# Kernel tuning notes

Measured on AMD Instinct MI355X. Metric: run time of the kernel, lower is better.

The kernel has to match this reference:

```python
import jax, jax.numpy as jnp
import numpy as np

RHO = 1e-8
EPS = 1e-8
THRESH = 0.9
MARK = -2


def maxi(x):
    # keep only the max entry along last dim, zero elsewhere
    idx = jnp.argmax(x, axis=-1, keepdims=True)
    return jnp.where(jnp.arange(x.shape[-1]) == idx, x, 0.0)


def argmaxi(x, eps=EPS):
    mx = jnp.abs(maxi(x))
    factors = jnp.max(mx, axis=-1, keepdims=True) - eps
    return mx / factors


def outer_forward(mm0, xs, rho=RHO):
    # mm0: (fields, mems, dim), xs: (batch, fields, dim)
    m = mm0 - 0.5
    x = xs - 0.5
    num = jnp.einsum('fmd,bfd->bfm', m, x) * 0.5
    m_norm = jnp.sqrt(jnp.sum(m * m, axis=-1))            # (f, m)
    x_norm = jnp.sqrt(jnp.sum(x * x, axis=-1))[..., None]  # (b, f, 1)
    return num / (m_norm[None] * x_norm + rho) + 0.5


def hidden_forward(mm, child_x, rho=RHO):
    # mm: (nodes, children, h_mems, c_mems), child_x: (batch, nodes*children, c_mems)
    n, c, hm, cm = mm.shape
    b = child_x.shape[0]
    x = maxi(child_x).reshape(b, n, c, cm)
    prop = jnp.einsum('nchk,bnck->bnh', mm, x)
    x_norm = jnp.sqrt(jnp.sum(x * x, axis=(2, 3)))[..., None]  # (b, n, 1)
    return prop / (c * x_norm + rho)


def mark_reserved_indices(acts, usages, trigger, mark=MARK):
    # acts: (b, n, m); usages: (n, m); trigger: (b, n, 1)
    res = jnp.argsort(acts, axis=-1)[:, :, -1:]        # argmax index, (b, n, 1)
    res = jnp.where(trigger, -1, res)
    res = res[:, :, 0].T                               # (n, b)
    sort_indices = jnp.argsort(usages, axis=-1)        # (n, m) ascending usage
    mask = res != -1                                   # (n, b)
    matches = ((res[:, :, None] == sort_indices[:, None, :]) & mask[:, :, None]).any(axis=1)  # (n, m)
    return jnp.where(matches, mark, sort_indices), sort_indices


def move_value_to_back(x, value=MARK):
    order = jnp.argsort((x == value).astype(jnp.int32), axis=-1)  # stable sort
    return jnp.take_along_axis(x, order, axis=-1)


def expand_for_batches(x, batch_size):
    n, m = x.shape
    full = batch_size // m + 1
    tiled = jnp.broadcast_to(x[None], (full, n, m)).transpose(1, 0, 2).reshape(n, -1)
    return tiled[:, :batch_size]


def growth_argmaxi(x, counts, eps=EPS, threshold=THRESH):
    b, n, m = x.shape
    normal = argmaxi(x, eps)
    trigger = jnp.sum(x > threshold, axis=-1, keepdims=True) <= 0  # (b, n, 1)
    avail, allidx = mark_reserved_indices(normal, counts, trigger, MARK)
    avail = move_value_to_back(avail, MARK)
    avail = expand_for_batches(avail, b)
    allidx = expand_for_batches(allidx, b)
    final = jnp.where(avail == MARK, allidx, avail)  # (n, b)
    idx = final.T.reshape(b, n, 1)
    vals = jnp.take_along_axis(x, idx, axis=-1)
    vals = jnp.where(vals == 0, 1.0, vals)
    gp = jnp.where(jnp.arange(m) == idx, vals, 0.0)  # scatter into zeros
    gp = argmaxi(jnp.abs(gp), eps)
    grown = jnp.where(trigger, gp, normal)
    uc = jnp.sum(grown, axis=0)
    uc = jnp.where(uc <= 0, counts, uc)
    return grown, uc


def setup_inputs() -> dict:
    key = jax.random.key(0)
    k1, k2, k3, k4 = jax.random.split(key, 4)
    xs = jax.random.uniform(k1, (32, 4096, 64), dtype=jnp.float32)
    mm0 = jax.random.uniform(k2, (4096, 64, 64), dtype=jnp.float32)
    mm1 = jax.random.normal(k3, (512, 8, 64, 64), dtype=jnp.float32) * 0.1
    mm2 = jax.random.normal(k4, (64, 8, 64, 64), dtype=jnp.float32) * 0.1
    counts = jnp.ones((64, 64), dtype=jnp.float32)
    return {'xs': xs, 'mm0': mm0, 'mm1': mm1, 'mm2': mm2, 'counts': counts}


def reference(xs, mm0, mm1, mm2, counts):
    h0 = outer_forward(mm0, xs)      # (b, 4096, 64)
    h1 = hidden_forward(mm1, h0)     # (b, 512, 64)
    h2 = hidden_forward(mm2, h1)     # (b, 64, 64)
    grown, _ = growth_argmaxi(h2, counts)
    return grown
```

## Files before the change

### kernel.cpp

```cpp
#include <hip/hip_runtime.h>
#include <cstdint>
#include <cstddef>

#define RHO 1e-8f
#define EPSV 1e-8f
#define THRESH 0.9f

typedef float v2f __attribute__((ext_vector_type(2)));

__device__ __forceinline__ float wave_max(float v) {
#pragma unroll
  for (int off = 1; off < 64; off <<= 1) v = fmaxf(v, __shfl_xor(v, off, 64));
  return v;
}

__device__ __forceinline__ void lds_barrier() {
  asm volatile("s_waitcnt lgkmcnt(0)" ::: "memory");
  __builtin_amdgcn_sched_barrier(0);
  __builtin_amdgcn_s_barrier();
  __builtin_amdgcn_sched_barrier(0);
}

__global__ __launch_bounds__(128) void stage1_kernel(
    const float* __restrict__ xs, const float* __restrict__ mm0,
    float* __restrict__ maxv1, int* __restrict__ idx1) {
  const int tid = threadIdx.x;
  const int lane = tid & 63;
  const int wave = tid >> 6;
  const int f = blockIdx.x;
  const int mg = lane >> 3, bg = lane & 7;
  const int mrow0 = wave * 32 + mg;

  __shared__ float bestS[2][32];
  __shared__ int bidxS[2][32];

  const float* mb = mm0 + (size_t)f * 4096 + (size_t)mrow0 * 64;
  const float* xb = xs + (size_t)f * 64 + (size_t)bg * (4096 * 64);

  v2f acc[4][4][2];
  v2f na[4], nx[4];
#pragma unroll
  for (int i = 0; i < 4; ++i) {
    na[i] = (v2f){0.f, 0.f};
    nx[i] = (v2f){0.f, 0.f};
#pragma unroll
    for (int j = 0; j < 4; ++j) {
      acc[i][j][0] = (v2f){0.f, 0.f};
      acc[i][j][1] = (v2f){0.f, 0.f};
    }
  }

#pragma clang loop unroll_count(2)
  for (int q = 0; q < 16; ++q) {
    float4 a[4], bx[4];
#pragma unroll
    for (int i = 0; i < 4; ++i) {
      float4 v = *reinterpret_cast<const float4*>(mb + i * (8 * 64) + 4 * q);
      a[i] = (float4){v.x - 0.5f, v.y - 0.5f, v.z - 0.5f, v.w - 0.5f};
    }
#pragma unroll
    for (int j = 0; j < 4; ++j) {
      float4 v = *reinterpret_cast<const float4*>(
          xb + (size_t)j * (8 * 4096 * 64) + 4 * q);
      bx[j] = (float4){v.x - 0.5f, v.y - 0.5f, v.z - 0.5f, v.w - 0.5f};
    }
#pragma unroll
    for (int i = 0; i < 4; ++i) {
      na[i] = (v2f){a[i].x, a[i].y} * (v2f){a[i].x, a[i].y} + na[i];
      na[i] = (v2f){a[i].z, a[i].w} * (v2f){a[i].z, a[i].w} + na[i];
    }
#pragma unroll
    for (int j = 0; j < 4; ++j) {
      nx[j] = (v2f){bx[j].x, bx[j].y} * (v2f){bx[j].x, bx[j].y} + nx[j];
      nx[j] = (v2f){bx[j].z, bx[j].w} * (v2f){bx[j].z, bx[j].w} + nx[j];
    }
#pragma unroll
    for (int i = 0; i < 4; ++i)
#pragma unroll
      for (int j = 0; j < 4; ++j) {
        acc[i][j][0] = (v2f){a[i].x, a[i].y} * (v2f){bx[j].x, bx[j].y} + acc[i][j][0];
        acc[i][j][1] = (v2f){a[i].z, a[i].w} * (v2f){bx[j].z, bx[j].w} + acc[i][j][1];
      }
  }

  float mn_i[4], xn_j[4];
#pragma unroll
  for (int i = 0; i < 4; ++i) mn_i[i] = sqrtf(na[i].x + na[i].y);
#pragma unroll
  for (int j = 0; j < 4; ++j) xn_j[j] = sqrtf(nx[j].x + nx[j].y);

  float best[4];
  int bidx[4];
#pragma unroll
  for (int j = 0; j < 4; ++j) { best[j] = -__builtin_inff(); bidx[j] = 0; }
#pragma unroll
  for (int i = 0; i < 4; ++i)
#pragma unroll
    for (int j = 0; j < 4; ++j) {
      const float dot =
          acc[i][j][0].x + acc[i][j][0].y + acc[i][j][1].x + acc[i][j][1].y;
      const float val = (dot * 0.5f) / (mn_i[i] * xn_j[j] + RHO) + 0.5f;
      if (val > best[j]) { best[j] = val; bidx[j] = mrow0 + 8 * i; }
    }
#pragma unroll
  for (int off = 8; off < 64; off <<= 1) {
#pragma unroll
    for (int j = 0; j < 4; ++j) {
      const float pv = __shfl_xor(best[j], off, 64);
      const int pm = __shfl_xor(bidx[j], off, 64);
      if (pv > best[j] || (pv == best[j] && pm < bidx[j])) {
        best[j] = pv; bidx[j] = pm;
      }
    }
  }
  if (mg == 0) {
#pragma unroll
    for (int j = 0; j < 4; ++j) {
      bestS[wave][bg + 8 * j] = best[j];
      bidxS[wave][bg + 8 * j] = bidx[j];
    }
  }
  __syncthreads();
  if (tid < 32) {
    const float v0 = bestS[0][tid], v1 = bestS[1][tid];
    const int i0 = bidxS[0][tid], i1 = bidxS[1][tid];
    const bool take1 = (v1 > v0);
    maxv1[f * 32 + tid] = take1 ? v1 : v0;
    idx1[f * 32 + tid] = take1 ? i1 : i0;
  }
}

#define STAGE_WRITE(T, R)                                    \
  do {                                                       \
    _Pragma("unroll") for (int i_ = 0; i_ < 4; ++i_) {       \
      const int g_ = tid + 256 * i_;                         \
      const int h_ = g_ >> 4, k0_ = (g_ & 15) * 4;           \
      (T)[(k0_ + 0) * 64 + (h_ ^ (k0_ + 0))] = (R)[i_].x;    \
      (T)[(k0_ + 1) * 64 + (h_ ^ (k0_ + 1))] = (R)[i_].y;    \
      (T)[(k0_ + 2) * 64 + (h_ ^ (k0_ + 2))] = (R)[i_].z;    \
      (T)[(k0_ + 3) * 64 + (h_ ^ (k0_ + 3))] = (R)[i_].w;    \
    }                                                        \
  } while (0)

#define LOAD_CHILD(R, C)                                     \
  do {                                                       \
    _Pragma("unroll") for (int i_ = 0; i_ < 4; ++i_)         \
        (R)[i_] = src[(C) * 1024 + tid + 256 * i_];          \
  } while (0)

#define COMPUTE_CHILD(C, T)                                              \
  do {                                                                   \
    _Pragma("unroll") for (int i_ = 0; i_ < 8; ++i_) {                   \
      const int b_ = wave * 8 + i_;                                      \
      const int k_ = ixL[(C) * 32 + b_];                                 \
      const float v_ = mvL[(C) * 32 + b_];                               \
      const float w_ = (T)[k_ * 64 + (lane ^ k_)];                       \
      acc[i_] = fmaf(w_, v_, acc[i_]);                                   \
      s2[i_] = fmaf(v_, v_, s2[i_]);                                     \
    }                                                                    \
  } while (0)

#define PIPELINE_MATMUL()                        \
  do {                                           \
    float4 rE[4], rO[4];                         \
    LOAD_CHILD(rE, 0);                           \
    LOAD_CHILD(rO, 1);                           \
    STAGE_WRITE(tA, rE);                         \
    lds_barrier();                               \
    _Pragma("unroll") for (int cc = 0; cc < 8; cc += 2) { \
      if (cc + 2 < 8) LOAD_CHILD(rE, cc + 2);    \
      COMPUTE_CHILD(cc, tA);                     \
      STAGE_WRITE(tB, rO);                       \
      lds_barrier();                             \
      if (cc + 3 < 8) LOAD_CHILD(rO, cc + 3);    \
      COMPUTE_CHILD(cc + 1, tB);                 \
      if (cc + 2 < 8) { STAGE_WRITE(tA, rE); }   \
      lds_barrier();                             \
    }                                            \
  } while (0)

__global__ __launch_bounds__(256) void stage2_kernel(
    const float* __restrict__ maxv_in, const int* __restrict__ idx_in,
    const float* __restrict__ mm,
    float* __restrict__ maxv_out, int* __restrict__ idx_out) {
  const int node = blockIdx.x;
  const int lane = threadIdx.x & 63;
  const int wave = threadIdx.x >> 6;
  const int tid = threadIdx.x;

  __shared__ float tA[4096], tB[4096];
  __shared__ float mvL[256];
  __shared__ int ixL[256];

  const float4* src = reinterpret_cast<const float4*>(mm + (size_t)node * (8 * 4096));

  mvL[tid] = maxv_in[node * 256 + tid];
  ixL[tid] = idx_in[node * 256 + tid];

  float acc[8], s2[8];
#pragma unroll
  for (int i = 0; i < 8; ++i) { acc[i] = 0.f; s2[i] = 0.f; }

  PIPELINE_MATMUL();

#pragma unroll
  for (int i = 0; i < 8; ++i) {
    const int b = wave * 8 + i;
    const float val = acc[i] / (8.f * sqrtf(s2[i]) + RHO);
    const float mx = wave_max(val);
    unsigned long long t = __ballot(val == mx);
    int j0 = __ffsll((long long)t) - 1;
    if (lane == 0) {
      maxv_out[node * 32 + b] = mx;
      idx_out[node * 32 + b] = j0;
    }
  }
}

__global__ __launch_bounds__(256) void grow_kernel(
    const float* __restrict__ maxv_in, const int* __restrict__ idx_in,
    const float* __restrict__ mm,
    const float* __restrict__ counts, float* __restrict__ out) {
  const int node = blockIdx.x;
  const int lane = threadIdx.x & 63;
  const int wave = threadIdx.x >> 6;
  const int tid = threadIdx.x;

  __shared__ float tA[4096], tB[4096];
  __shared__ float mvL[256];
  __shared__ int ixL[256];
  __shared__ float hbuf[32 * 64];
  __shared__ float mxvS[32];
  __shared__ int idxS[32];
  __shared__ int trgS[32];
  __shared__ float cntS[64];
  __shared__ int sidxS[64];
  __shared__ int flagS[64];
  __shared__ int compS[64];
  __shared__ int selS[32];
  __shared__ float valS[32];
  __shared__ int keptS[1];

  const float4* src = reinterpret_cast<const float4*>(mm + (size_t)node * (8 * 4096));

  mvL[tid] = maxv_in[node * 256 + tid];
  ixL[tid] = idx_in[node * 256 + tid];

  float acc[8], s2[8];
#pragma unroll
  for (int i = 0; i < 8; ++i) { acc[i] = 0.f; s2[i] = 0.f; }

  PIPELINE_MATMUL();

#pragma unroll
  for (int i = 0; i < 8; ++i) {
    const int b = wave * 8 + i;
    const float val = acc[i] / (8.f * sqrtf(s2[i]) + RHO);
    const float mx = wave_max(val);
    unsigned long long t = __ballot(val == mx);
    int j0 = __ffsll((long long)t) - 1;
    hbuf[b * 64 + lane] = val;
    unsigned long long big = __ballot(val > THRESH);
    if (lane == 0) {
      mxvS[b] = mx; idxS[b] = j0; trgS[b] = (big == 0ULL) ? 1 : 0;
    }
  }

  if (tid < 64) { cntS[tid] = counts[node * 64 + tid]; flagS[tid] = 0; }
  __syncthreads();
  if (tid < 64) {
    float cl = cntS[tid];
    int rank = 0;
    for (int j = 0; j < 64; ++j) {
      float cj = cntS[j];
      rank += (cj < cl || (cj == cl && j < tid)) ? 1 : 0;
    }
    sidxS[rank] = tid;
  }
  __syncthreads();
  if (tid < 32) {
    const int b = tid;
    if (!trgS[b]) {
      int j = idxS[b];
      float a = fabsf(mxvS[b]);
      int res;
      if (a > EPSV) res = j;
      else if (a == 0.f) res = 63;
      else if (a == EPSV) res = j;
      else res = (j == 63) ? 62 : 63;
      flagS[res] = 1;
    }
  }
  __syncthreads();
  if (wave == 0) {
    int s = sidxS[lane];
    int keep = flagS[s] ? 0 : 1;
    unsigned long long kb = __ballot(keep);
    int pos = __popcll(kb & ((1ULL << lane) - 1ULL));
    if (keep) compS[pos] = s;
    if (lane == 0) keptS[0] = __popcll(kb);
  }
  __syncthreads();
  if (tid < 32) {
    const int b = tid;
    int fin = (b < keptS[0]) ? compS[b] : sidxS[b];
    int idxb; float a;
    if (trgS[b]) {
      idxb = fin;
      float v = hbuf[b * 64 + idxb];
      if (v == 0.f) v = 1.f;
      a = fabsf(v);
    } else {
      idxb = idxS[b];
      a = fabsf(mxvS[b]);
    }
    selS[b] = idxb;
    valS[b] = a / (a - EPSV);
  }
  __syncthreads();
#pragma unroll
  for (int r = 0; r < 8; ++r) {
    int i = tid + 256 * r;
    int b = i >> 6, h = i & 63;
    out[((size_t)b * 64 + node) * 64 + h] = (h == selS[b]) ? valS[b] : 0.f;
  }
}

extern "C" void kernel_launch(void* const* d_in, const int* in_sizes, int n_in,
                              void* d_out, int out_size, void* d_ws, size_t ws_size,
                              hipStream_t stream) {
  const float* xs = (const float*)d_in[0];
  const float* mm0 = (const float*)d_in[1];
  const float* mm1 = (const float*)d_in[2];
  const float* mm2 = (const float*)d_in[3];
  const float* counts = (const float*)d_in[4];
  float* out = (float*)d_out;
  char* ws = (char*)d_ws;

  float* maxv1 = (float*)(ws + 0);
  int* idx1 = (int*)(ws + 524288);
  float* maxv2 = (float*)(ws + 1048576);
  int* idx2 = (int*)(ws + 1114112);

  stage1_kernel<<<dim3(4096), dim3(128), 0, stream>>>(xs, mm0, maxv1, idx1);
  stage2_kernel<<<dim3(512), dim3(256), 0, stream>>>(maxv1, idx1, mm1, maxv2, idx2);
  grow_kernel<<<dim3(64), dim3(256), 0, stream>>>(maxv2, idx2, mm2, counts, out);
}
```

Measured before the change: 247.3 us.

## Stage mm0 and xs through swizzled LDS with register prefetch, four fields per block

Stage1 now processes four fields per block. For each field it copies the 64x64 mm0 tile and the 32x64 xs slice into XOR-swizzled shared memory, with the next field's tiles prefetched into registers and double-buffered so global loads overlap compute. Previously each thread read its operands straight from global memory with strided float4 loads. The per-block argmax reduction is also remapped so each wave owns 16 batches and writes results directly, removing the cross-wave LDS merge. This costs more LDS (about 24KB), more registers, extra barriers, and four times fewer blocks.

```diff
diff --git a/kernel.cpp b/kernel.cpp
--- a/kernel.cpp
+++ b/kernel.cpp
@@ -27,107 +27,181 @@
   const int tid = threadIdx.x;
   const int lane = tid & 63;
   const int wave = tid >> 6;
-  const int f = blockIdx.x;
-  const int mg = lane >> 3, bg = lane & 7;
-  const int mrow0 = wave * 32 + mg;
-
-  __shared__ float bestS[2][32];
-  __shared__ int bidxS[2][32];
-
-  const float* mb = mm0 + (size_t)f * 4096 + (size_t)mrow0 * 64;
-  const float* xb = xs + (size_t)f * 64 + (size_t)bg * (4096 * 64);
-
-  v2f acc[4][4][2];
-  v2f na[4], nx[4];
-#pragma unroll
-  for (int i = 0; i < 4; ++i) {
-    na[i] = (v2f){0.f, 0.f};
-    nx[i] = (v2f){0.f, 0.f};
+  const int mg = lane & 15, bg = lane >> 4;
+
+  __shared__ float mS[2][4096];
+  __shared__ float xS[2048];
+
+  const int f0 = blockIdx.x * 4;
+
+  float4 Rm[8], Rx[4];
+
+#define S1_LOADM(F)                                                      \
+  do {                                                                   \
+    const float* mf_ = mm0 + (size_t)(F)*4096;                           \
+    _Pragma("unroll") for (int i_ = 0; i_ < 8; ++i_) {                   \
+      const int g_ = tid + 128 * i_;                                     \
+      Rm[i_] = *reinterpret_cast<const float4*>(mf_ + g_ * 4);           \
+    }                                                                    \
+  } while (0)
+
+#define S1_LOADX(F)                                                      \
+  do {                                                                   \
+    _Pragma("unroll") for (int i_ = 0; i_ < 4; ++i_) {                   \
+      const int g_ = tid + 128 * i_;                                     \
+      const int b_ = g_ >> 4, q_ = g_ & 15;                              \
+      Rx[i_] = *reinterpret_cast<const float4*>(                         \
+          xs + ((size_t)b_ * 4096 + (F)) * 64 + q_ * 4);                 \
+    }                                                                    \
+  } while (0)
+
+#define S1_WRITEM(P)                                                     \
+  do {                                                                   \
+    _Pragma("unroll") for (int i_ = 0; i_ < 8; ++i_) {                   \
+      const int g_ = tid + 128 * i_;                                     \
+      const int r_ = g_ >> 4, q_ = g_ & 15;                              \
+      float4 w_ = {Rm[i_].x - 0.5f, Rm[i_].y - 0.5f, Rm[i_].z - 0.5f,    \
+                   Rm[i_].w - 0.5f};                                     \
+      *reinterpret_cast<float4*>(                                        \
+          &mS[P][(r_ * 16 + (q_ ^ (r_ & 15))) * 4]) = w_;                \
+    }                                                                    \
+  } while (0)
+
+#define S1_WRITEX()                                                      \
+  do {                                                                   \
+    _Pragma("unroll") for (int i_ = 0; i_ < 4; ++i_) {                   \
+      const int g_ = tid + 128 * i_;                                     \
+      const int b_ = g_ >> 4, q_ = g_ & 15;                              \
+      float4 w_ = {Rx[i_].x - 0.5f, Rx[i_].y - 0.5f, Rx[i_].z - 0.5f,    \
+                   Rx[i_].w - 0.5f};                                     \
+      *reinterpret_cast<float4*>(                                        \
+          &xS[(b_ * 16 + (q_ ^ (b_ & 15))) * 4]) = w_;                   \
+    }                                                                    \
+  } while (0)
+
+  S1_LOADM(f0);
+  S1_LOADX(f0);
+  S1_WRITEM(0);
+  S1_WRITEX();
+  S1_LOADM(f0 + 1);
+  S1_LOADX(f0 + 1);
+  lds_barrier();
+
+#pragma unroll
+  for (int k = 0; k < 4; ++k) {
+    const int f = f0 + k;
+    const float* mT = mS[k & 1];
+
+    v2f acc[4][4][2];
+    v2f na[4], nx[4];
+#pragma unroll
+    for (int i = 0; i < 4; ++i) {
+      na[i] = (v2f){0.f, 0.f};
+      nx[i] = (v2f){0.f, 0.f};
+#pragma unroll
+      for (int j = 0; j < 4; ++j) {
+        acc[i][j][0] = (v2f){0.f, 0.f};
+        acc[i][j][1] = (v2f){0.f, 0.f};
+      }
+    }
+
+#pragma unroll
+    for (int q = 0; q < 16; ++q) {
+      float4 a[4], bx[4];
+#pragma unroll
+      for (int i = 0; i < 4; ++i) {
+        const int r = mg + 16 * i;
+        a[i] = *reinterpret_cast<const float4*>(
+            &mT[(r * 16 + (q ^ (r & 15))) * 4]);
+      }
+#pragma unroll
+      for (int j = 0; j < 4; ++j) {
+        const int b = wave * 16 + bg + 4 * j;
+        bx[j] = *reinterpret_cast<const float4*>(
+            &xS[(b * 16 + (q ^ (b & 15))) * 4]);
+      }
+#pragma unroll
+      for (int i = 0; i < 4; ++i) {
+        na[i] = (v2f){a[i].x, a[i].y} * (v2f){a[i].x, a[i].y} + na[i];
+        na[i] = (v2f){a[i].z, a[i].w} * (v2f){a[i].z, a[i].w} + na[i];
+      }
+#pragma unroll
+      for (int j = 0; j < 4; ++j) {
+        nx[j] = (v2f){bx[j].x, bx[j].y} * (v2f){bx[j].x, bx[j].y} + nx[j];
+        nx[j] = (v2f){bx[j].z, bx[j].w} * (v2f){bx[j].z, bx[j].w} + nx[j];
+      }
+#pragma unroll
+      for (int i = 0; i < 4; ++i)
+#pragma unroll
+        for (int j = 0; j < 4; ++j) {
+          acc[i][j][0] =
+              (v2f){a[i].x, a[i].y} * (v2f){bx[j].x, bx[j].y} + acc[i][j][0];
+          acc[i][j][1] =
+              (v2f){a[i].z, a[i].w} * (v2f){bx[j].z, bx[j].w} + acc[i][j][1];
+        }
+    }
+
+    if (k < 3) S1_WRITEM((k + 1) & 1);
+
+    float mn_i[4], xn_j[4];
+#pragma unroll
+    for (int i = 0; i < 4; ++i) mn_i[i] = sqrtf(na[i].x + na[i].y);
+#pragma unroll
+    for (int j = 0; j < 4; ++j) xn_j[j] = sqrtf(nx[j].x + nx[j].y);
+
+    float best[4];
+    int bidx[4];
 #pragma unroll
     for (int j = 0; j < 4; ++j) {
-      acc[i][j][0] = (v2f){0.f, 0.f};
-      acc[i][j][1] = (v2f){0.f, 0.f};
-    }
-  }
-
-#pragma clang loop unroll_count(2)
-  for (int q = 0; q < 16; ++q) {
-    float4 a[4], bx[4];
-#pragma unroll
-    for (int i = 0; i < 4; ++i) {
-      float4 v = *reinterpret_cast<const float4*>(mb + i * (8 * 64) + 4 * q);
-      a[i] = (float4){v.x - 0.5f, v.y - 0.5f, v.z - 0.5f, v.w - 0.5f};
-    }
-#pragma unroll
-    for (int j = 0; j < 4; ++j) {
-      float4 v = *reinterpret_cast<const float4*>(
-          xb + (size_t)j * (8 * 4096 * 64) + 4 * q);
-      bx[j] = (float4){v.x - 0.5f, v.y - 0.5f, v.z - 0.5f, v.w - 0.5f};
-    }
-#pragma unroll
-    for (int i = 0; i < 4; ++i) {
-      na[i] = (v2f){a[i].x, a[i].y} * (v2f){a[i].x, a[i].y} + na[i];
-      na[i] = (v2f){a[i].z, a[i].w} * (v2f){a[i].z, a[i].w} + na[i];
-    }
-#pragma unroll
-    for (int j = 0; j < 4; ++j) {
-      nx[j] = (v2f){bx[j].x, bx[j].y} * (v2f){bx[j].x, bx[j].y} + nx[j];
-      nx[j] = (v2f){bx[j].z, bx[j].w} * (v2f){bx[j].z, bx[j].w} + nx[j];
+      best[j] = -__builtin_inff();
+      bidx[j] = 0;
     }
 #pragma unroll
     for (int i = 0; i < 4; ++i)
 #pragma unroll
       for (int j = 0; j < 4; ++j) {
-        acc[i][j][0] = (v2f){a[i].x, a[i].y} * (v2f){bx[j].x, bx[j].y} + acc[i][j][0];
-        acc[i][j][1] = (v2f){a[i].z, a[i].w} * (v2f){bx[j].z, bx[j].w} + acc[i][j][1];
-      }
-  }
-
-  float mn_i[4], xn_j[4];
-#pragma unroll
-  for (int i = 0; i < 4; ++i) mn_i[i] = sqrtf(na[i].x + na[i].y);
-#pragma unroll
-  for (int j = 0; j < 4; ++j) xn_j[j] = sqrtf(nx[j].x + nx[j].y);
-
-  float best[4];
-  int bidx[4];
-#pragma unroll
-  for (int j = 0; j < 4; ++j) { best[j] = -__builtin_inff(); bidx[j] = 0; }
-#pragma unroll
-  for (int i = 0; i < 4; ++i)
-#pragma unroll
-    for (int j = 0; j < 4; ++j) {
-      const float dot =
-          acc[i][j][0].x + acc[i][j][0].y + acc[i][j][1].x + acc[i][j][1].y;
-      const float val = (dot * 0.5f) / (mn_i[i] * xn_j[j] + RHO) + 0.5f;
-      if (val > best[j]) { best[j] = val; bidx[j] = mrow0 + 8 * i; }
-    }
-#pragma unroll
-  for (int off = 8; off < 64; off <<= 1) {
-#pragma unroll
-    for (int j = 0; j < 4; ++j) {
-      const float pv = __shfl_xor(best[j], off, 64);
-      const int pm = __shfl_xor(bidx[j], off, 64);
-      if (pv > best[j] || (pv == best[j] && pm < bidx[j])) {
-        best[j] = pv; bidx[j] = pm;
-      }
-    }
-  }
-  if (mg == 0) {
-#pragma unroll
-    for (int j = 0; j < 4; ++j) {
-      bestS[wave][bg + 8 * j] = best[j];
-      bidxS[wave][bg + 8 * j] = bidx[j];
-    }
-  }
-  __syncthreads();
-  if (tid < 32) {
-    const float v0 = bestS[0][tid], v1 = bestS[1][tid];
-    const int i0 = bidxS[0][tid], i1 = bidxS[1][tid];
-    const bool take1 = (v1 > v0);
-    maxv1[f * 32 + tid] = take1 ? v1 : v0;
-    idx1[f * 32 + tid] = take1 ? i1 : i0;
-  }
+        const float dot =
+            acc[i][j][0].x + acc[i][j][0].y + acc[i][j][1].x + acc[i][j][1].y;
+        const float val = (dot * 0.5f) / (mn_i[i] * xn_j[j] + RHO) + 0.5f;
+        if (val > best[j]) {
+          best[j] = val;
+          bidx[j] = mg + 16 * i;
+        }
+      }
+#pragma unroll
+    for (int off = 1; off < 16; off <<= 1) {
+#pragma unroll
+      for (int j = 0; j < 4; ++j) {
+        const float pv = __shfl_xor(best[j], off, 64);
+        const int pm = __shfl_xor(bidx[j], off, 64);
+        if (pv > best[j] || (pv == best[j] && pm < bidx[j])) {
+          best[j] = pv;
+          bidx[j] = pm;
+        }
+      }
+    }
+
+    if (k < 3) lds_barrier();
+    if (k < 3) S1_WRITEX();
+    if (k < 2) {
+      S1_LOADM(f0 + k + 2);
+      S1_LOADX(f0 + k + 2);
+    }
+    if (mg == 0) {
+#pragma unroll
+      for (int j = 0; j < 4; ++j) {
+        const int b = wave * 16 + bg + 4 * j;
+        maxv1[f * 32 + b] = best[j];
+        idx1[f * 32 + b] = bidx[j];
+      }
+    }
+    if (k < 3) lds_barrier();
+  }
+
+#undef S1_LOADM
+#undef S1_LOADX
+#undef S1_WRITEM
+#undef S1_WRITEX
 }
 
 #define STAGE_WRITE(T, R)                                    \
@@ -342,7 +416,7 @@
   float* maxv2 = (float*)(ws + 1048576);
   int* idx2 = (int*)(ws + 1114112);
 
-  stage1_kernel<<<dim3(4096), dim3(128), 0, stream>>>(xs, mm0, maxv1, idx1);
+  stage1_kernel<<<dim3(1024), dim3(128), 0, stream>>>(xs, mm0, maxv1, idx1);
   stage2_kernel<<<dim3(512), dim3(256), 0, stream>>>(maxv1, idx1, mm1, maxv2, idx2);
   grow_kernel<<<dim3(64), dim3(256), 0, stream>>>(maxv2, idx2, mm2, counts, out);
 }
```

Result: faster. 231.3 us (-6.5%).

## Stage mm0 and xs tiles into LDS via async global_load_lds with XOR swizzle

Applied to the files above, without the earlier changes.

Stage 1 now copies each field's 64x64 mm0 block and its 32x64 xs slice into shared memory using direct global-to-LDS loads, with an XOR swizzle to avoid bank conflicts. Row norms are computed once per row by dedicated threads instead of redundantly inside the dot-product loop. The main loop then reads operands from LDS instead of issuing strided global float4 loads. This adds an up-front load phase with two barriers and about 25KB of LDS per block, which may reduce occupancy and serialize load and compute.

```diff
diff --git a/kernel.cpp b/kernel.cpp
--- a/kernel.cpp
+++ b/kernel.cpp
@@ -19,6 +19,12 @@
   __builtin_amdgcn_sched_barrier(0);
   __builtin_amdgcn_s_barrier();
   __builtin_amdgcn_sched_barrier(0);
+}
+
+__device__ __forceinline__ void gll16(const float* gp, float* lp) {
+  __builtin_amdgcn_global_load_lds(
+      (const __attribute__((address_space(1))) void*)gp,
+      (__attribute__((address_space(3))) void*)lp, 16, 0, 0);
 }
 
 __global__ __launch_bounds__(128) void stage1_kernel(
@@ -28,51 +34,75 @@
   const int lane = tid & 63;
   const int wave = tid >> 6;
   const int f = blockIdx.x;
+
+  __shared__ float mS[64 * 64];
+  __shared__ float xS[32 * 64];
+  __shared__ float mnS[64];
+  __shared__ float xnS[32];
+  __shared__ float bestS[2][32];
+  __shared__ int bidxS[2][32];
+
+  const float* mf = mm0 + (size_t)f * 4096;
+#pragma unroll
+  for (int i = 0; i < 8; ++i) {
+    const int s = i * 128 + tid;
+    const int r = s >> 4;
+    const int q = (s & 15) ^ (r & 15);
+    gll16(mf + (r * 16 + q) * 4, &mS[(i * 128 + wave * 64) * 4]);
+  }
+  const float* xf = xs + (size_t)f * 64;
+#pragma unroll
+  for (int i = 0; i < 4; ++i) {
+    const int s = i * 128 + tid;
+    const int b = s >> 4;
+    const int q = (s & 15) ^ (b & 15);
+    gll16(xf + (size_t)b * (4096 * 64) + q * 4, &xS[(i * 128 + wave * 64) * 4]);
+  }
+  __syncthreads();
+
+  if (tid < 96) {
+    const int r = (tid < 64) ? tid : (tid - 64);
+    const float* base = (tid < 64) ? mS : xS;
+    v2f s = {0.f, 0.f};
+#pragma unroll
+    for (int q = 0; q < 16; ++q) {
+      float4 v = *reinterpret_cast<const float4*>(&base[(r * 16 + (q ^ (r & 15))) * 4]);
+      v2f p0 = {v.x - 0.5f, v.y - 0.5f};
+      v2f p1 = {v.z - 0.5f, v.w - 0.5f};
+      s = p0 * p0 + s;
+      s = p1 * p1 + s;
+    }
+    const float n = sqrtf(s.x + s.y);
+    if (tid < 64) mnS[r] = n; else xnS[r] = n;
+  }
+  __syncthreads();
+
   const int mg = lane >> 3, bg = lane & 7;
   const int mrow0 = wave * 32 + mg;
-
-  __shared__ float bestS[2][32];
-  __shared__ int bidxS[2][32];
-
-  const float* mb = mm0 + (size_t)f * 4096 + (size_t)mrow0 * 64;
-  const float* xb = xs + (size_t)f * 64 + (size_t)bg * (4096 * 64);
-
   v2f acc[4][4][2];
-  v2f na[4], nx[4];
-#pragma unroll
-  for (int i = 0; i < 4; ++i) {
-    na[i] = (v2f){0.f, 0.f};
-    nx[i] = (v2f){0.f, 0.f};
+#pragma unroll
+  for (int i = 0; i < 4; ++i)
 #pragma unroll
     for (int j = 0; j < 4; ++j) {
       acc[i][j][0] = (v2f){0.f, 0.f};
       acc[i][j][1] = (v2f){0.f, 0.f};
     }
-  }
-
-#pragma clang loop unroll_count(2)
-  for (int q = 0; q < 16; ++q) {
+
+#pragma unroll
+  for (int d0 = 0; d0 < 64; d0 += 4) {
+    const int q = d0 >> 2;
     float4 a[4], bx[4];
 #pragma unroll
     for (int i = 0; i < 4; ++i) {
-      float4 v = *reinterpret_cast<const float4*>(mb + i * (8 * 64) + 4 * q);
+      const int r = mrow0 + 8 * i;
+      float4 v = *reinterpret_cast<const float4*>(&mS[(r * 16 + (q ^ (r & 15))) * 4]);
       a[i] = (float4){v.x - 0.5f, v.y - 0.5f, v.z - 0.5f, v.w - 0.5f};
     }
 #pragma unroll
     for (int j = 0; j < 4; ++j) {
-      float4 v = *reinterpret_cast<const float4*>(
-          xb + (size_t)j * (8 * 4096 * 64) + 4 * q);
+      const int b = bg + 8 * j;
+      float4 v = *reinterpret_cast<const float4*>(&xS[(b * 16 + (q ^ (b & 15))) * 4]);
       bx[j] = (float4){v.x - 0.5f, v.y - 0.5f, v.z - 0.5f, v.w - 0.5f};
-    }
-#pragma unroll
-    for (int i = 0; i < 4; ++i) {
-      na[i] = (v2f){a[i].x, a[i].y} * (v2f){a[i].x, a[i].y} + na[i];
-      na[i] = (v2f){a[i].z, a[i].w} * (v2f){a[i].z, a[i].w} + na[i];
-    }
-#pragma unroll
-    for (int j = 0; j < 4; ++j) {
-      nx[j] = (v2f){bx[j].x, bx[j].y} * (v2f){bx[j].x, bx[j].y} + nx[j];
-      nx[j] = (v2f){bx[j].z, bx[j].w} * (v2f){bx[j].z, bx[j].w} + nx[j];
     }
 #pragma unroll
     for (int i = 0; i < 4; ++i)
@@ -85,9 +115,9 @@
 
   float mn_i[4], xn_j[4];
 #pragma unroll
-  for (int i = 0; i < 4; ++i) mn_i[i] = sqrtf(na[i].x + na[i].y);
-#pragma unroll
-  for (int j = 0; j < 4; ++j) xn_j[j] = sqrtf(nx[j].x + nx[j].y);
+  for (int i = 0; i < 4; ++i) mn_i[i] = mnS[mrow0 + 8 * i];
+#pragma unroll
+  for (int j = 0; j < 4; ++j) xn_j[j] = xnS[bg + 8 * j];
 
   float best[4];
   int bidx[4];
```

New measurement: 207.2 us. 1.19x faster.
